# Performance work log

Measured on AMD Instinct MI355X. Metric: run time of the kernel, lower is better.

The kernel has to match this reference:

```python
import jax, jax.numpy as jnp
import numpy as np
from jax import lax

TD_MAX = 2000
STRIDE = 100


def setup_inputs() -> dict:
    key = jax.random.key(0)
    x = jax.random.normal(key, (20000, 512, 3), dtype=jnp.float32)
    return {"x": x}


def reference(x) -> jnp.ndarray:
    # x: [T, N, 3] trajectory (2D input would be reshaped to [T, -1, 3])
    if x.ndim == 2:
        x = x.reshape(x.shape[0], -1, 3)
    T = x.shape[0]
    N3 = x.shape[1] * x.shape[2]
    t0s = jnp.arange(0, T - TD_MAX, STRIDE)  # time origins, stride 100

    def step(msd, t0):
        # window of td_max frames starting at t0: [td_max, N, 3]
        w = lax.dynamic_slice(x, (t0, 0, 0), (TD_MAX, x.shape[1], x.shape[2]))
        d = w - w[0]                       # displacement from origin frame
        msd = msd + jnp.sum(d * d, axis=(1, 2)) / N3
        return msd, None

    msd0 = jnp.zeros((TD_MAX,), dtype=x.dtype)
    msd, _ = lax.scan(step, msd0, t0s)
    return msd / t0s.shape[0]
```

## Files before the change

### kernel.cpp

```cpp
#include <hip/hip_runtime.h>


typedef __attribute__((ext_vector_type(8))) short bf16x8;
typedef __attribute__((ext_vector_type(4))) float f32x4;

#define ROWF   1536
#define NFRAME 20000
#define NORIG  180
#define WIN    20
#define FB     32
#define NFB    625
#define NKS    48
#define SLOTS  640
#define TDMAX  2000
#define SCALE  (1.0f / (1536.0f * 180.0f))

static __device__ __forceinline__ short f2bf(float f) {
    unsigned u = __builtin_bit_cast(unsigned, f);
    u += 0x7fffu + ((u >> 16) & 1u);
    return (short)(u >> 16);
}

static __device__ __forceinline__ bf16x8 pack8(const float4& v0, const float4& v1) {
    bf16x8 r;
    r[0] = f2bf(v0.x); r[1] = f2bf(v0.y); r[2] = f2bf(v0.z); r[3] = f2bf(v0.w);
    r[4] = f2bf(v1.x); r[5] = f2bf(v1.y); r[6] = f2bf(v1.z); r[7] = f2bf(v1.w);
    return r;
}

static __device__ __forceinline__ float sum8sq(const float4& v0, const float4& v1) {
    return v0.x*v0.x + v0.y*v0.y + v0.z*v0.z + v0.w*v0.w
         + v1.x*v1.x + v1.y*v1.y + v1.z*v1.z + v1.w*v1.w;
}

__global__ __launch_bounds__(256)
void msd_dot_kernel(const float* __restrict__ x, float* __restrict__ ws) {
    __shared__ float sS[FB];
    __shared__ float sO[32];

    const int b    = blockIdx.x;
    const int t0   = b * FB;
    const int lane = threadIdx.x & 63;
    const int w    = threadIdx.x >> 6;
    const int mt   = w >> 1;
    const int nt   = w & 1;
    const int m    = lane & 15;
    const int quad = lane >> 4;

    const int cmin = t0 / 100;
    int iBase = cmin - (WIN - 1); if (iBase < 0) iBase = 0;

    const int t    = t0 + 16 * mt + m;
    const int iNom = iBase + 16 * nt + m;
    const int iClp = (iNom < NORIG) ? iNom : (NORIG - 1);

    const float* pA = x + (size_t)t * ROWF + quad * 8;
    const float* pB = x + (size_t)(iClp * 100) * ROWF + quad * 8;

    f32x4 acc = {};
    float sAp = 0.0f, sBp = 0.0f;

    #pragma unroll 2
    for (int ks = 0; ks < NKS; ++ks) {
        const float4 a0 = *(const float4*)(pA + ks * 32);
        const float4 a1 = *(const float4*)(pA + ks * 32 + 4);
        const float4 b0 = *(const float4*)(pB + ks * 32);
        const float4 b1 = *(const float4*)(pB + ks * 32 + 4);
        sAp += sum8sq(a0, a1);
        sBp += sum8sq(b0, b1);
        acc = __builtin_amdgcn_mfma_f32_16x16x32_bf16(pack8(a0, a1), pack8(b0, b1),
                                                      acc, 0, 0, 0);
    }

    sAp += __shfl_xor(sAp, 16, 64); sAp += __shfl_xor(sAp, 32, 64);
    sBp += __shfl_xor(sBp, 16, 64); sBp += __shfl_xor(sBp, 32, 64);
    if (lane < 16) { sS[16 * mt + m] = sAp; sO[16 * nt + m] = sBp; }
    __syncthreads();

    float* wsb = ws + (size_t)b * SLOTS;
    #pragma unroll
    for (int r = 0; r < 4; ++r) {
        const int j  = 16 * mt + quad * 4 + r;
        const int tt = t0 + j;
        const int c  = tt / 100;
        const int i  = iBase + 16 * nt + m;
        const int k  = c - i;
        if (k >= 0 && k < WIN && i < NORIG) {
            wsb[k * FB + j] = sS[j] + sO[16 * nt + m] - 2.0f * acc[r];
        }
    }
}

__global__ __launch_bounds__(256)
void msd_reduce_kernel(const float* __restrict__ ws, float* __restrict__ out) {
    const int td = blockIdx.x * 256 + threadIdx.x;
    if (td >= TDMAX) return;
    const int k  = td / 100;
    float acc = 0.0f;
    for (int i = 0; i < NORIG; ++i) {
        const int t = 100 * i + td;
        acc += ws[(size_t)(t >> 5) * SLOTS + k * FB + (t & 31)];
    }
    out[td] = acc * SCALE;
}

extern "C" void kernel_launch(void* const* d_in, const int* in_sizes, int n_in,
                              void* d_out, int out_size, void* d_ws, size_t ws_size,
                              hipStream_t stream) {
    const float* x = (const float*)d_in[0];
    float* out = (float*)d_out;
    float* ws  = (float*)d_ws;

    msd_dot_kernel<<<NFB, 256, 0, stream>>>(x, ws);
    msd_reduce_kernel<<<(TDMAX + 255) / 256, 256, 0, stream>>>(ws, out);
}
```

Before: 210.5 us.

## Split K dimension across two blocks and parallelize reduction per lag

Each frame block's dot-product work is split across two blocks along the 1536-wide feature dimension, doubling grid size from 625 to 1250 blocks so more of the GPU is occupied. Each half writes partial results to its own workspace slot. The reduce kernel now adds both partials and uses one 64-lane wave per lag with a shuffle reduction, replacing a single thread per lag that looped serially over 180 origins. This roughly doubles workspace traffic and adds a second read per element in the reduction.

```diff
diff --git a/kernel.cpp b/kernel.cpp
--- a/kernel.cpp
+++ b/kernel.cpp
@@ -10,7 +10,9 @@
 #define WIN    20
 #define FB     32
 #define NFB    625
-#define NKS    48
+#define NKC    2
+#define KC     768
+#define NKS    24
 #define SLOTS  640
 #define TDMAX  2000
 #define SCALE  (1.0f / (1536.0f * 180.0f))
@@ -38,8 +40,9 @@
     __shared__ float sS[FB];
     __shared__ float sO[32];
 
-    const int b    = blockIdx.x;
-    const int t0   = b * FB;
+    const int fb   = blockIdx.x >> 1;
+    const int kc   = blockIdx.x & 1;
+    const int t0   = fb * FB;
     const int lane = threadIdx.x & 63;
     const int w    = threadIdx.x >> 6;
     const int mt   = w >> 1;
@@ -54,13 +57,13 @@
     const int iNom = iBase + 16 * nt + m;
     const int iClp = (iNom < NORIG) ? iNom : (NORIG - 1);
 
-    const float* pA = x + (size_t)t * ROWF + quad * 8;
-    const float* pB = x + (size_t)(iClp * 100) * ROWF + quad * 8;
+    const float* pA = x + (size_t)t * ROWF + kc * KC + quad * 8;
+    const float* pB = x + (size_t)(iClp * 100) * ROWF + kc * KC + quad * 8;
 
     f32x4 acc = {};
     float sAp = 0.0f, sBp = 0.0f;
 
-    #pragma unroll 2
+    #pragma unroll 4
     for (int ks = 0; ks < NKS; ++ks) {
         const float4 a0 = *(const float4*)(pA + ks * 32);
         const float4 a1 = *(const float4*)(pA + ks * 32 + 4);
@@ -77,7 +80,7 @@
     if (lane < 16) { sS[16 * mt + m] = sAp; sO[16 * nt + m] = sBp; }
     __syncthreads();
 
-    float* wsb = ws + (size_t)b * SLOTS;
+    float* wsb = ws + (size_t)blockIdx.x * SLOTS;
     #pragma unroll
     for (int r = 0; r < 4; ++r) {
         const int j  = 16 * mt + quad * 4 + r;
@@ -91,17 +94,25 @@
     }
 }
 
-__global__ __launch_bounds__(256)
+__global__ __launch_bounds__(64)
 void msd_reduce_kernel(const float* __restrict__ ws, float* __restrict__ out) {
-    const int td = blockIdx.x * 256 + threadIdx.x;
-    if (td >= TDMAX) return;
-    const int k  = td / 100;
+    const int td   = blockIdx.x;
+    const int lane = threadIdx.x;
+    const int k    = td / 100;
+
     float acc = 0.0f;
-    for (int i = 0; i < NORIG; ++i) {
-        const int t = 100 * i + td;
-        acc += ws[(size_t)(t >> 5) * SLOTS + k * FB + (t & 31)];
+    #pragma unroll 1
+    for (int i = lane; i < NORIG; i += 64) {
+        const int t  = 100 * i + td;
+        const int fb = t >> 5;
+        const int sl = k * FB + (t & 31);
+        acc += ws[(size_t)(fb * 2 + 0) * SLOTS + sl];
+        acc += ws[(size_t)(fb * 2 + 1) * SLOTS + sl];
     }
-    out[td] = acc * SCALE;
+    #pragma unroll
+    for (int off = 32; off >= 1; off >>= 1)
+        acc += __shfl_xor(acc, off, 64);
+    if (lane == 0) out[td] = acc * SCALE;
 }
 
 extern "C" void kernel_launch(void* const* d_in, const int* in_sizes, int n_in,
@@ -111,6 +122,6 @@
     float* out = (float*)d_out;
     float* ws  = (float*)d_ws;
 
-    msd_dot_kernel<<<NFB, 256, 0, stream>>>(x, ws);
-    msd_reduce_kernel<<<(TDMAX + 255) / 256, 256, 0, stream>>>(ws, out);
+    msd_dot_kernel<<<NFB * NKC, 256, 0, stream>>>(x, ws);
+    msd_reduce_kernel<<<TDMAX, 64, 0, stream>>>(ws, out);
 }
```

After: 203.1 us. -3.5%, faster.
